# Performance work log

Hardware: AMD Instinct MI355X
Metric: run time of the kernel (lower is better)

## Reference

```python
import jax, jax.numpy as jnp
import numpy as np
from jax import lax

DN = ('NHWC', 'HWIO', 'NHWC')
EPS = 1e-7


def squash(s, axis=-1):
    sq = jnp.sum(s * s, axis=axis, keepdims=True)
    return s * (sq / (1.0 + sq) / jnp.sqrt(sq + EPS))


def setup_inputs() -> dict:
    key = jax.random.key(0)
    ks = jax.random.split(key, 4)
    inputs = jax.random.normal(ks[0], (2, 250, 250, 3), dtype=jnp.float32)
    conv_w = jax.random.normal(ks[1], (9, 9, 3, 256), dtype=jnp.float32) * 0.02
    conv_b = jnp.zeros((256,), dtype=jnp.float32)
    pc_w = jax.random.normal(ks[2], (9, 9, 256, 128), dtype=jnp.float32) * 0.02
    pc_b = jnp.zeros((128,), dtype=jnp.float32)
    # CapsLayer routing weights: [num_caps=8, in_caps=219024, dim_caps=8, in_dim=8]
    W_caps = jax.random.normal(ks[3], (8, 219024, 8, 8), dtype=jnp.float32) * 0.05
    return {"inputs": inputs, "conv_w": conv_w, "conv_b": conv_b,
            "pc_w": pc_w, "pc_b": pc_b, "W_caps": W_caps}


def reference(inputs, conv_w, conv_b, pc_w, pc_b, W_caps):
    ROUTINGS = 3
    B = inputs.shape[0]
    # Conv backbone: 250x250x3 -> 242x242x256, ReLU
    x = lax.conv_general_dilated(inputs, conv_w, (1, 1), 'VALID', dimension_numbers=DN)
    x = jax.nn.relu(x + conv_b)
    # PrimaryCaps: linear conv (128 ch, k=9, s=2, valid) -> 117x117x128 -> [B, 219024, 8] -> squash
    pc = lax.conv_general_dilated(x, pc_w, (2, 2), 'VALID', dimension_numbers=DN) + pc_b
    u = squash(pc.reshape(B, -1, 8))  # [B, N=219024, 8]
    # Prediction vectors u_hat[b,j,i,o] = W[j,i,o,d] u[b,i,d]
    u_hat = jnp.einsum('jiod,bid->bjio', W_caps, u)  # [B, J, N, 8]
    J, N = W_caps.shape[0], W_caps.shape[1]
    b_logits = jnp.zeros((B, J, N), dtype=u_hat.dtype)
    v = None
    for r in range(ROUTINGS):
        c = jax.nn.softmax(b_logits, axis=1)          # coupling over output caps
        s = jnp.einsum('bji,bjio->bjo', c, u_hat)     # [B, J, 8]
        v = squash(s)
        if r < ROUTINGS - 1:
            b_logits = b_logits + jnp.einsum('bjo,bjio->bji', v, u_hat)
    return v  # [B, 8, 8]
```

## Files before the change

### kernel.cpp

```cpp
#include <hip/hip_runtime.h>

#define N_CAPS 219024
#define J_CAPS 8

typedef __attribute__((ext_vector_type(8))) __bf16 bf16x8;
typedef __attribute__((ext_vector_type(4))) float  f32x4;
typedef __attribute__((ext_vector_type(8))) short  short8;

__device__ __forceinline__ unsigned short f2bf(float f) {
    unsigned int u = __float_as_uint(f);
    u = (u + 0x7FFFu + ((u >> 16) & 1u)) >> 16;
    return (unsigned short)u;
}

__global__ __launch_bounds__(256) void conv1_kernel(
    const float* __restrict__ in, const float* __restrict__ w,
    const float* __restrict__ bias, unsigned short* __restrict__ out)
{
    const int oc  = threadIdx.x;
    const int ox0 = blockIdx.x * 16;
    const int oy  = blockIdx.y;
    const int b   = blockIdx.z;

    __shared__ float lin[9][24][3];
    for (int idx = threadIdx.x; idx < 9 * 24 * 3; idx += 256) {
        int r   = idx / (24 * 3);
        int rem = idx - r * (24 * 3);
        int col = rem / 3;
        int c   = rem - col * 3;
        int iy  = oy + r;
        int ix  = ox0 + col;
        float v = 0.f;
        if (ix < 250) v = in[((b * 250 + iy) * 250 + ix) * 3 + c];
        lin[r][col][c] = v;
    }
    __syncthreads();

    float acc[16];
#pragma unroll
    for (int t = 0; t < 16; ++t) acc[t] = 0.f;

    for (int ky = 0; ky < 9; ++ky) {
#pragma unroll
        for (int ic = 0; ic < 3; ++ic) {
            float xv[24];
#pragma unroll
            for (int c2 = 0; c2 < 24; ++c2) xv[c2] = lin[ky][c2][ic];
#pragma unroll
            for (int kx = 0; kx < 9; ++kx) {
                float wv = w[((ky * 9 + kx) * 3 + ic) * 256 + oc];
#pragma unroll
                for (int t = 0; t < 16; ++t)
                    acc[t] += xv[kx + t] * wv;
            }
        }
    }

    float bv = bias[oc];
#pragma unroll
    for (int t = 0; t < 16; ++t) {
        int ox = ox0 + t;
        if (ox < 242) {
            float v = acc[t] + bv;
            out[((b * 242 + oy) * 242 + ox) * 256 + oc] = f2bf(v > 0.f ? v : 0.f);
        }
    }
}

__global__ __launch_bounds__(256) void w2_convert_kernel(
    const float* __restrict__ w, unsigned short* __restrict__ wt)
{
    int idx = blockIdx.x * 256 + threadIdx.x;
    if (idx >= 81 * 128 * 256) return;
    int ic = idx & 255;
    int t  = idx >> 8;
    int oc = t & 127;
    int p  = t >> 7;
    wt[idx] = f2bf(w[(p * 256 + ic) * 128 + oc]);
}

__global__ __launch_bounds__(256) void conv2_mfma_kernel(
    const unsigned short* __restrict__ x1bf,
    const unsigned short* __restrict__ w2t,
    const float* __restrict__ bias,
    float* __restrict__ out)
{
    const int bx   = blockIdx.x;
    const int oy   = blockIdx.y;
    const int b    = blockIdx.z;
    const int tid  = threadIdx.x;
    const int wave = tid >> 6;
    const int lane = tid & 63;
    const int li   = lane & 15;
    const int quad = lane >> 4;
    const int wn   = wave * 32;
    const int ox0  = bx * 64;

    __shared__ __align__(16) unsigned short As[135 * 128];

    f32x4 acc[4][2];
#pragma unroll
    for (int mt = 0; mt < 4; ++mt) {
        acc[mt][0] = (f32x4){0.f, 0.f, 0.f, 0.f};
        acc[mt][1] = (f32x4){0.f, 0.f, 0.f, 0.f};
    }

    const int n0 = wn + li;
    const int n1 = wn + 16 + li;
    const size_t bofs0 = (size_t)n0 * 256 + quad * 8;
    const size_t bofs1 = (size_t)n1 * 256 + quad * 8;

    for (int ky = 0; ky < 9; ++ky) {
        const int iy = 2 * oy + ky;
        const unsigned short* xrow =
            x1bf + ((size_t)(b * 242 + iy) * 242 + 2 * ox0) * 256;

        for (int hq = 0; hq < 2; ++hq) {
            __syncthreads();
            for (int it = 0; it < 9; ++it) {
                int ct = it * 256 + tid;
                if (ct < 135 * 16) {
                    int col = ct >> 4;
                    int cc  = ct & 15;
                    int src = cc ^ ((col >> 1) & 7);
                    *(short8*)&As[ct * 8] =
                        *(const short8*)&xrow[col * 256 + hq * 128 + src * 8];
                }
            }
            __syncthreads();

            const size_t bo0 = bofs0 + hq * 128;
            const size_t bo1 = bofs1 + hq * 128;

            for (int kx = 0; kx < 9; ++kx) {
                const unsigned short* wp = w2t + ((size_t)(ky * 9 + kx) << 15);
                const int colbase = (li << 1) + kx;
                const int sw = (li + (kx >> 1)) & 7;
                const unsigned short* abase = As + colbase * 128;
#pragma unroll
                for (int kc = 0; kc < 4; ++kc) {
                    bf16x8 b0 = *(const bf16x8*)&wp[bo0 + kc * 32];
                    bf16x8 b1 = *(const bf16x8*)&wp[bo1 + kc * 32];
                    const int chs = ((kc << 2) + quad) ^ sw;
#pragma unroll
                    for (int mt = 0; mt < 4; ++mt) {
                        bf16x8 a = *(const bf16x8*)&abase[mt * 4096 + chs * 8];
                        acc[mt][0] = __builtin_amdgcn_mfma_f32_16x16x32_bf16(a, b0, acc[mt][0], 0, 0, 0);
                        acc[mt][1] = __builtin_amdgcn_mfma_f32_16x16x32_bf16(a, b1, acc[mt][1], 0, 0, 0);
                    }
                }
            }
        }
    }

    const float bv0 = bias[n0];
    const float bv1 = bias[n1];
#pragma unroll
    for (int mt = 0; mt < 4; ++mt) {
#pragma unroll
        for (int r = 0; r < 4; ++r) {
            const int m  = mt * 16 + quad * 4 + r;
            const int ox = ox0 + m;
            if (ox < 117) {
                float* op = &out[((size_t)(b * 117 + oy) * 117 + ox) * 128];
                op[n0] = acc[mt][0][r] + bv0;
                op[n1] = acc[mt][1][r] + bv1;
            }
        }
    }
}

__global__ __launch_bounds__(256) void squash_u_kernel(float* data, int n_groups)
{
    int i = blockIdx.x * 256 + threadIdx.x;
    if (i >= n_groups) return;
    float4* p = (float4*)(data + (size_t)i * 8);
    float4 a = p[0], c = p[1];
    float sq = a.x * a.x + a.y * a.y + a.z * a.z + a.w * a.w
             + c.x * c.x + c.y * c.y + c.z * c.z + c.w * c.w;
    float scale = (sq / (1.f + sq)) * rsqrtf(sq + 1e-7f);
    p[0] = make_float4(a.x * scale, a.y * scale, a.z * scale, a.w * scale);
    p[1] = make_float4(c.x * scale, c.y * scale, c.z * scale, c.w * scale);
}

__global__ __launch_bounds__(256) void uhat_kernel(
    const float* __restrict__ W, const float* __restrict__ u,
    float* __restrict__ uhat)
{
    int idx = blockIdx.x * 256 + threadIdx.x;
    if (idx >= J_CAPS * N_CAPS) return;
    int j = idx / N_CAPS;
    int i = idx - j * N_CAPS;

    const float4* wp = (const float4*)(W + (size_t)idx * 64);
    const float4* u0 = (const float4*)(u + (size_t)i * 8);
    const float4* u1 = (const float4*)(u + ((size_t)N_CAPS + i) * 8);
    float4 u0a = u0[0], u0b = u0[1];
    float4 u1a = u1[0], u1b = u1[1];

    float o0[8], o1[8];
#pragma unroll
    for (int o = 0; o < 8; ++o) {
        float4 wa = wp[2 * o], wb = wp[2 * o + 1];
        o0[o] = wa.x * u0a.x + wa.y * u0a.y + wa.z * u0a.z + wa.w * u0a.w
              + wb.x * u0b.x + wb.y * u0b.y + wb.z * u0b.z + wb.w * u0b.w;
        o1[o] = wa.x * u1a.x + wa.y * u1a.y + wa.z * u1a.z + wa.w * u1a.w
              + wb.x * u1b.x + wb.y * u1b.y + wb.z * u1b.z + wb.w * u1b.w;
    }
    float4* d0 = (float4*)(uhat + ((size_t)(0 * J_CAPS + j) * N_CAPS + i) * 8);
    float4* d1 = (float4*)(uhat + ((size_t)(1 * J_CAPS + j) * N_CAPS + i) * 8);
    d0[0] = make_float4(o0[0], o0[1], o0[2], o0[3]);
    d0[1] = make_float4(o0[4], o0[5], o0[6], o0[7]);
    d1[0] = make_float4(o1[0], o1[1], o1[2], o1[3]);
    d1[1] = make_float4(o1[4], o1[5], o1[6], o1[7]);
}

template <int MODE>
__global__ __launch_bounds__(256) void routing_kernel(
    const float* __restrict__ uhat, const float* __restrict__ vprev,
    const float* __restrict__ b_in, float* __restrict__ b_out,
    float* __restrict__ s)
{
    const int bb = blockIdx.y;
    __shared__ float vsh[64];
    __shared__ float ssh[64];
    if (threadIdx.x < 64) {
        ssh[threadIdx.x] = 0.f;
        vsh[threadIdx.x] = (MODE > 0) ? vprev[bb * 64 + threadIdx.x] : 0.f;
    }
    __syncthreads();

    float acc[64];
#pragma unroll
    for (int k = 0; k < 64; ++k) acc[k] = 0.f;

    const float* ub = uhat + (size_t)bb * J_CAPS * (size_t)N_CAPS * 8;
    for (int i = blockIdx.x * 256 + threadIdx.x; i < N_CAPS; i += gridDim.x * 256) {
        float uh[64];
#pragma unroll
        for (int j = 0; j < 8; ++j) {
            const float* p = ub + ((size_t)j * N_CAPS + i) * 8;
            float4 x0 = *(const float4*)p;
            float4 x1 = *(const float4*)(p + 4);
            uh[j * 8 + 0] = x0.x; uh[j * 8 + 1] = x0.y;
            uh[j * 8 + 2] = x0.z; uh[j * 8 + 3] = x0.w;
            uh[j * 8 + 4] = x1.x; uh[j * 8 + 5] = x1.y;
            uh[j * 8 + 6] = x1.z; uh[j * 8 + 7] = x1.w;
        }
        float c[8];
        if (MODE == 0) {
#pragma unroll
            for (int j = 0; j < 8; ++j) c[j] = 0.125f;
        } else {
            float bj[8];
#pragma unroll
            for (int j = 0; j < 8; ++j) {
                float d = 0.f;
#pragma unroll
                for (int o = 0; o < 8; ++o) d += vsh[j * 8 + o] * uh[j * 8 + o];
                bj[j] = d;
            }
            if (MODE == 2) {
#pragma unroll
                for (int j = 0; j < 8; ++j)
                    bj[j] += b_in[((size_t)bb * 8 + j) * N_CAPS + i];
            } else {
#pragma unroll
                for (int j = 0; j < 8; ++j)
                    b_out[((size_t)bb * 8 + j) * N_CAPS + i] = bj[j];
            }
            float m = bj[0];
#pragma unroll
            for (int j = 1; j < 8; ++j) m = fmaxf(m, bj[j]);
            float se = 0.f;
#pragma unroll
            for (int j = 0; j < 8; ++j) { c[j] = __expf(bj[j] - m); se += c[j]; }
            float inv = 1.f / se;
#pragma unroll
            for (int j = 0; j < 8; ++j) c[j] *= inv;
        }
#pragma unroll
        for (int k = 0; k < 64; ++k) acc[k] += c[k >> 3] * uh[k];
    }

#pragma unroll
    for (int k = 0; k < 64; ++k) {
        float v = acc[k];
        for (int off = 32; off > 0; off >>= 1)
            v += __shfl_down(v, off, 64);
        if ((threadIdx.x & 63) == 0) atomicAdd(&ssh[k], v);
    }
    __syncthreads();
    if (threadIdx.x < 64) atomicAdd(&s[bb * 64 + threadIdx.x], ssh[threadIdx.x]);
}

__global__ void squash_v_kernel(const float* __restrict__ s, float* __restrict__ v)
{
    int t = threadIdx.x;
    if (t >= 16) return;
    const float4* p = (const float4*)(s + t * 8);
    float4 a = p[0], c = p[1];
    float sq = a.x * a.x + a.y * a.y + a.z * a.z + a.w * a.w
             + c.x * c.x + c.y * c.y + c.z * c.z + c.w * c.w;
    float scale = (sq / (1.f + sq)) * rsqrtf(sq + 1e-7f);
    float4* d = (float4*)(v + t * 8);
    d[0] = make_float4(a.x * scale, a.y * scale, a.z * scale, a.w * scale);
    d[1] = make_float4(c.x * scale, c.y * scale, c.z * scale, c.w * scale);
}

__global__ void zero_kernel(float* p, int n)
{
    int i = blockIdx.x * 256 + threadIdx.x;
    if (i < n) p[i] = 0.f;
}

extern "C" void kernel_launch(void* const* d_in, const int* in_sizes, int n_in,
                              void* d_out, int out_size, void* d_ws, size_t ws_size,
                              hipStream_t stream)
{
    const float* in = (const float*)d_in[0];
    const float* w1 = (const float*)d_in[1];
    const float* b1 = (const float*)d_in[2];
    const float* w2 = (const float*)d_in[3];
    const float* b2 = (const float*)d_in[4];
    const float* Wc = (const float*)d_in[5];
    float* out = (float*)d_out;
    char* wsb  = (char*)d_ws;

    float*          uhat = (float*)wsb;
    unsigned short* x1bf = (unsigned short*)wsb;
    float*          pc   = (float*)(wsb + 112140288);
    float*          blog = (float*)(wsb + 126157824);
    unsigned short* w2t  = (unsigned short*)(wsb + 140175360);
    float*          sbuf = (float*)(wsb + 145483776);
    float*          vbuf = (float*)(wsb + 145484288);

    w2_convert_kernel<<<(81 * 128 * 256 + 255) / 256, 256, 0, stream>>>(w2, w2t);
    conv1_kernel<<<dim3(16, 242, 2), 256, 0, stream>>>(in, w1, b1, x1bf);
    conv2_mfma_kernel<<<dim3(2, 117, 2), 256, 0, stream>>>(x1bf, w2t, b2, pc);
    squash_u_kernel<<<(2 * N_CAPS + 255) / 256, 256, 0, stream>>>(pc, 2 * N_CAPS);
    uhat_kernel<<<(J_CAPS * N_CAPS + 255) / 256, 256, 0, stream>>>(Wc, pc, uhat);

    zero_kernel<<<1, 128, 0, stream>>>(sbuf, 128);
    routing_kernel<0><<<dim3(256, 2), 256, 0, stream>>>(uhat, nullptr, nullptr, nullptr, sbuf);
    squash_v_kernel<<<1, 64, 0, stream>>>(sbuf, vbuf);

    zero_kernel<<<1, 128, 0, stream>>>(sbuf, 128);
    routing_kernel<1><<<dim3(256, 2), 256, 0, stream>>>(uhat, vbuf, nullptr, blog, sbuf);
    squash_v_kernel<<<1, 64, 0, stream>>>(sbuf, vbuf);

    zero_kernel<<<1, 128, 0, stream>>>(sbuf, 128);
    routing_kernel<2><<<dim3(256, 2), 256, 0, stream>>>(uhat, vbuf, blog, nullptr, sbuf);
    squash_v_kernel<<<1, 64, 0, stream>>>(sbuf, out);
}
```

Measured before the change: 1.305 ms.

## Split conv2 reduction over ky into three partials and widen per-wave N tile

```diff
diff --git a/kernel.cpp b/kernel.cpp
--- a/kernel.cpp
+++ b/kernel.cpp
@@ -79,13 +79,14 @@
     wt[idx] = f2bf(w[(p * 256 + ic) * 128 + oc]);
 }
 
-__global__ __launch_bounds__(256) void conv2_mfma_kernel(
+__global__ __launch_bounds__(128, 2) void conv2_mfma_kernel(
     const unsigned short* __restrict__ x1bf,
     const unsigned short* __restrict__ w2t,
-    const float* __restrict__ bias,
-    float* __restrict__ out)
+    float* __restrict__ part)
 {
     const int bx   = blockIdx.x;
+    const int oxt  = bx & 1;
+    const int kys  = bx >> 1;
     const int oy   = blockIdx.y;
     const int b    = blockIdx.z;
     const int tid  = threadIdx.x;
@@ -93,32 +94,34 @@
     const int lane = tid & 63;
     const int li   = lane & 15;
     const int quad = lane >> 4;
-    const int wn   = wave * 32;
-    const int ox0  = bx * 64;
+    const int wn   = wave * 64;
+    const int ox0  = oxt * 64;
+    const int ky0  = kys * 3;
 
     __shared__ __align__(16) unsigned short As[135 * 128];
 
-    f32x4 acc[4][2];
-#pragma unroll
-    for (int mt = 0; mt < 4; ++mt) {
-        acc[mt][0] = (f32x4){0.f, 0.f, 0.f, 0.f};
-        acc[mt][1] = (f32x4){0.f, 0.f, 0.f, 0.f};
-    }
-
-    const int n0 = wn + li;
-    const int n1 = wn + 16 + li;
-    const size_t bofs0 = (size_t)n0 * 256 + quad * 8;
-    const size_t bofs1 = (size_t)n1 * 256 + quad * 8;
-
-    for (int ky = 0; ky < 9; ++ky) {
+    f32x4 acc[4][4];
+#pragma unroll
+    for (int mt = 0; mt < 4; ++mt)
+#pragma unroll
+        for (int nt = 0; nt < 4; ++nt)
+            acc[mt][nt] = (f32x4){0.f, 0.f, 0.f, 0.f};
+
+    size_t bofs[4];
+#pragma unroll
+    for (int nt = 0; nt < 4; ++nt)
+        bofs[nt] = (size_t)(wn + nt * 16 + li) * 256 + quad * 8;
+
+    for (int kk = 0; kk < 3; ++kk) {
+        const int ky = ky0 + kk;
         const int iy = 2 * oy + ky;
         const unsigned short* xrow =
             x1bf + ((size_t)(b * 242 + iy) * 242 + 2 * ox0) * 256;
 
         for (int hq = 0; hq < 2; ++hq) {
             __syncthreads();
-            for (int it = 0; it < 9; ++it) {
-                int ct = it * 256 + tid;
+            for (int it = 0; it < 17; ++it) {
+                int ct = it * 128 + tid;
                 if (ct < 135 * 16) {
                     int col = ct >> 4;
                     int cc  = ct & 15;
@@ -129,58 +132,82 @@
             }
             __syncthreads();
 
-            const size_t bo0 = bofs0 + hq * 128;
-            const size_t bo1 = bofs1 + hq * 128;
-
             for (int kx = 0; kx < 9; ++kx) {
-                const unsigned short* wp = w2t + ((size_t)(ky * 9 + kx) << 15);
-                const int colbase = (li << 1) + kx;
+                const unsigned short* wp =
+                    w2t + ((size_t)(ky * 9 + kx) << 15) + hq * 128;
                 const int sw = (li + (kx >> 1)) & 7;
-                const unsigned short* abase = As + colbase * 128;
+                const unsigned short* abase = As + (2 * li + kx) * 128;
 #pragma unroll
                 for (int kc = 0; kc < 4; ++kc) {
-                    bf16x8 b0 = *(const bf16x8*)&wp[bo0 + kc * 32];
-                    bf16x8 b1 = *(const bf16x8*)&wp[bo1 + kc * 32];
+                    bf16x8 bfr[4];
+#pragma unroll
+                    for (int nt = 0; nt < 4; ++nt)
+                        bfr[nt] = *(const bf16x8*)&wp[bofs[nt] + kc * 32];
                     const int chs = ((kc << 2) + quad) ^ sw;
+                    __builtin_amdgcn_s_setprio(1);
 #pragma unroll
                     for (int mt = 0; mt < 4; ++mt) {
                         bf16x8 a = *(const bf16x8*)&abase[mt * 4096 + chs * 8];
-                        acc[mt][0] = __builtin_amdgcn_mfma_f32_16x16x32_bf16(a, b0, acc[mt][0], 0, 0, 0);
-                        acc[mt][1] = __builtin_amdgcn_mfma_f32_16x16x32_bf16(a, b1, acc[mt][1], 0, 0, 0);
+#pragma unroll
+                        for (int nt = 0; nt < 4; ++nt)
+                            acc[mt][nt] = __builtin_amdgcn_mfma_f32_16x16x32_bf16(
+                                a, bfr[nt], acc[mt][nt], 0, 0, 0);
                     }
+                    __builtin_amdgcn_s_setprio(0);
                 }
             }
         }
     }
 
-    const float bv0 = bias[n0];
-    const float bv1 = bias[n1];
+    float* pp = part + (size_t)kys * (2ull * 117 * 117 * 128)
+              + (size_t)(b * 117 + oy) * 117 * 128;
 #pragma unroll
     for (int mt = 0; mt < 4; ++mt) {
 #pragma unroll
         for (int r = 0; r < 4; ++r) {
-            const int m  = mt * 16 + quad * 4 + r;
-            const int ox = ox0 + m;
+            const int ox = ox0 + mt * 16 + quad * 4 + r;
             if (ox < 117) {
-                float* op = &out[((size_t)(b * 117 + oy) * 117 + ox) * 128];
-                op[n0] = acc[mt][0][r] + bv0;
-                op[n1] = acc[mt][1][r] + bv1;
-            }
-        }
-    }
-}
-
-__global__ __launch_bounds__(256) void squash_u_kernel(float* data, int n_groups)
-{
-    int i = blockIdx.x * 256 + threadIdx.x;
-    if (i >= n_groups) return;
-    float4* p = (float4*)(data + (size_t)i * 8);
-    float4 a = p[0], c = p[1];
-    float sq = a.x * a.x + a.y * a.y + a.z * a.z + a.w * a.w
-             + c.x * c.x + c.y * c.y + c.z * c.z + c.w * c.w;
+                float* op = pp + (size_t)ox * 128 + li;
+                op[wn]      = acc[mt][0][r];
+                op[wn + 16] = acc[mt][1][r];
+                op[wn + 32] = acc[mt][2][r];
+                op[wn + 48] = acc[mt][3][r];
+            }
+        }
+    }
+}
+
+__global__ __launch_bounds__(256) void squash_u_kernel(
+    const float* __restrict__ part, const float* __restrict__ bias,
+    float* __restrict__ u, int n_groups)
+{
+    int g = blockIdx.x * 256 + threadIdx.x;
+    if (g >= n_groups) return;
+    const size_t PSZ = 2ull * 117 * 117 * 128;
+    const float4* p0 = (const float4*)(part + (size_t)g * 8);
+    const float4* p1 = (const float4*)(part + PSZ + (size_t)g * 8);
+    const float4* p2 = (const float4*)(part + 2 * PSZ + (size_t)g * 8);
+    const float4* bp = (const float4*)(bias + (g & 15) * 8);
+    float4 a0 = p0[0], c0 = p0[1];
+    float4 a1 = p1[0], c1 = p1[1];
+    float4 a2 = p2[0], c2 = p2[1];
+    float4 ba = bp[0], bc = bp[1];
+    float x[8];
+    x[0] = a0.x + a1.x + a2.x + ba.x;
+    x[1] = a0.y + a1.y + a2.y + ba.y;
+    x[2] = a0.z + a1.z + a2.z + ba.z;
+    x[3] = a0.w + a1.w + a2.w + ba.w;
+    x[4] = c0.x + c1.x + c2.x + bc.x;
+    x[5] = c0.y + c1.y + c2.y + bc.y;
+    x[6] = c0.z + c1.z + c2.z + bc.z;
+    x[7] = c0.w + c1.w + c2.w + bc.w;
+    float sq = 0.f;
+#pragma unroll
+    for (int j = 0; j < 8; ++j) sq += x[j] * x[j];
     float scale = (sq / (1.f + sq)) * rsqrtf(sq + 1e-7f);
-    p[0] = make_float4(a.x * scale, a.y * scale, a.z * scale, a.w * scale);
-    p[1] = make_float4(c.x * scale, c.y * scale, c.z * scale, c.w * scale);
+    float4* d = (float4*)(u + (size_t)g * 8);
+    d[0] = make_float4(x[0] * scale, x[1] * scale, x[2] * scale, x[3] * scale);
+    d[1] = make_float4(x[4] * scale, x[5] * scale, x[6] * scale, x[7] * scale);
 }
 
 __global__ __launch_bounds__(256) void uhat_kernel(
@@ -327,18 +354,19 @@
     float* out = (float*)d_out;
     char* wsb  = (char*)d_ws;
 
-    float*          uhat = (float*)wsb;
-    unsigned short* x1bf = (unsigned short*)wsb;
-    float*          pc   = (float*)(wsb + 112140288);
-    float*          blog = (float*)(wsb + 126157824);
-    unsigned short* w2t  = (unsigned short*)(wsb + 140175360);
-    float*          sbuf = (float*)(wsb + 145483776);
-    float*          vbuf = (float*)(wsb + 145484288);
+    float*          uhat   = (float*)wsb;
+    unsigned short* x1bf   = (unsigned short*)wsb;
+    float*          pcpart = (float*)(wsb + 59969536);
+    float*          pc     = (float*)(wsb + 112140288);
+    float*          blog   = (float*)(wsb + 126157824);
+    unsigned short* w2t    = (unsigned short*)(wsb + 140175360);
+    float*          sbuf   = (float*)(wsb + 145483776);
+    float*          vbuf   = (float*)(wsb + 145484288);
 
     w2_convert_kernel<<<(81 * 128 * 256 + 255) / 256, 256, 0, stream>>>(w2, w2t);
     conv1_kernel<<<dim3(16, 242, 2), 256, 0, stream>>>(in, w1, b1, x1bf);
-    conv2_mfma_kernel<<<dim3(2, 117, 2), 256, 0, stream>>>(x1bf, w2t, b2, pc);
-    squash_u_kernel<<<(2 * N_CAPS + 255) / 256, 256, 0, stream>>>(pc, 2 * N_CAPS);
+    conv2_mfma_kernel<<<dim3(6, 117, 2), 128, 0, stream>>>(x1bf, w2t, pcpart);
+    squash_u_kernel<<<(2 * N_CAPS + 255) / 256, 256, 0, stream>>>(pcpart, b2, pc, 2 * N_CAPS);
     uhat_kernel<<<(J_CAPS * N_CAPS + 255) / 256, 256, 0, stream>>>(Wc, pc, uhat);
 
     zero_kernel<<<1, 128, 0, stream>>>(sbuf, 128);
```

After: 1.397 ms. +7.1%, slower.

## Double-buffer conv2 input tiles with async global-to-LDS loads

Applied to the files above, without the earlier changes.

```diff
diff --git a/kernel.cpp b/kernel.cpp
--- a/kernel.cpp
+++ b/kernel.cpp
@@ -6,6 +6,9 @@
 typedef __attribute__((ext_vector_type(8))) __bf16 bf16x8;
 typedef __attribute__((ext_vector_type(4))) float  f32x4;
 typedef __attribute__((ext_vector_type(8))) short  short8;
+
+typedef const __attribute__((address_space(1))) unsigned int gld_t;
+typedef __attribute__((address_space(3))) unsigned int lds_t;
 
 __device__ __forceinline__ unsigned short f2bf(float f) {
     unsigned int u = __float_as_uint(f);
@@ -79,7 +82,7 @@
     wt[idx] = f2bf(w[(p * 256 + ic) * 128 + oc]);
 }
 
-__global__ __launch_bounds__(256) void conv2_mfma_kernel(
+__global__ __launch_bounds__(256, 4) void conv2_mfma_kernel(
     const unsigned short* __restrict__ x1bf,
     const unsigned short* __restrict__ w2t,
     const float* __restrict__ bias,
@@ -96,7 +99,7 @@
     const int wn   = wave * 32;
     const int ox0  = bx * 64;
 
-    __shared__ __align__(16) unsigned short As[135 * 128];
+    __shared__ __align__(16) unsigned short As[2][135 * 64];
 
     f32x4 acc[4][2];
 #pragma unroll
@@ -110,47 +113,58 @@
     const size_t bofs0 = (size_t)n0 * 256 + quad * 8;
     const size_t bofs1 = (size_t)n1 * 256 + quad * 8;
 
-    for (int ky = 0; ky < 9; ++ky) {
-        const int iy = 2 * oy + ky;
-        const unsigned short* xrow =
-            x1bf + ((size_t)(b * 242 + iy) * 242 + 2 * ox0) * 256;
-
-        for (int hq = 0; hq < 2; ++hq) {
-            __syncthreads();
-            for (int it = 0; it < 9; ++it) {
-                int ct = it * 256 + tid;
-                if (ct < 135 * 16) {
-                    int col = ct >> 4;
-                    int cc  = ct & 15;
-                    int src = cc ^ ((col >> 1) & 7);
-                    *(short8*)&As[ct * 8] =
-                        *(const short8*)&xrow[col * 256 + hq * 128 + src * 8];
+    const unsigned short* xbase =
+        x1bf + ((size_t)(b * 242 + 2 * oy) * 242 + 2 * ox0) * 256;
+
+    auto stage = [&](int p) {
+        const int ky = p >> 2;
+        const int q  = p & 3;
+        const unsigned short* xr = xbase + (size_t)ky * (242 * 256) + q * 64;
+        unsigned short* db = &As[p & 1][0];
+#pragma unroll
+        for (int it = 0; it < 5; ++it) {
+            int ct = it * 256 + tid;
+            if (ct < 135 * 8) {
+                int col = ct >> 3;
+                int cc  = ct & 7;
+                int src = cc ^ ((col >> 1) & 7);
+                __builtin_amdgcn_global_load_lds(
+                    (gld_t*)(xr + (size_t)col * 256 + src * 8),
+                    (lds_t*)(db + (size_t)(it * 256 + wave * 64) * 8),
+                    16, 0, 0);
+            }
+        }
+    };
+
+    stage(0);
+    __syncthreads();
+
+    for (int p = 0; p < 36; ++p) {
+        if (p < 35) stage(p + 1);
+
+        const int ky = p >> 2;
+        const int q  = p & 3;
+        const unsigned short* asb = As[p & 1];
+
+        for (int kx = 0; kx < 9; ++kx) {
+            const unsigned short* wp =
+                w2t + ((size_t)(ky * 9 + kx) << 15) + q * 64;
+            const int sw = (li + (kx >> 1)) & 7;
+            const int colb = 2 * li + kx;
+#pragma unroll
+            for (int kc = 0; kc < 2; ++kc) {
+                bf16x8 b0 = *(const bf16x8*)&wp[bofs0 + kc * 32];
+                bf16x8 b1 = *(const bf16x8*)&wp[bofs1 + kc * 32];
+                const int c4 = ((kc << 2) + quad) ^ sw;
+#pragma unroll
+                for (int mt = 0; mt < 4; ++mt) {
+                    bf16x8 a = *(const bf16x8*)&asb[(size_t)(mt * 32 + colb) * 64 + c4 * 8];
+                    acc[mt][0] = __builtin_amdgcn_mfma_f32_16x16x32_bf16(a, b0, acc[mt][0], 0, 0, 0);
+                    acc[mt][1] = __builtin_amdgcn_mfma_f32_16x16x32_bf16(a, b1, acc[mt][1], 0, 0, 0);
                 }
             }
-            __syncthreads();
-
-            const size_t bo0 = bofs0 + hq * 128;
-            const size_t bo1 = bofs1 + hq * 128;
-
-            for (int kx = 0; kx < 9; ++kx) {
-                const unsigned short* wp = w2t + ((size_t)(ky * 9 + kx) << 15);
-                const int colbase = (li << 1) + kx;
-                const int sw = (li + (kx >> 1)) & 7;
-                const unsigned short* abase = As + colbase * 128;
-#pragma unroll
-                for (int kc = 0; kc < 4; ++kc) {
-                    bf16x8 b0 = *(const bf16x8*)&wp[bo0 + kc * 32];
-                    bf16x8 b1 = *(const bf16x8*)&wp[bo1 + kc * 32];
-                    const int chs = ((kc << 2) + quad) ^ sw;
-#pragma unroll
-                    for (int mt = 0; mt < 4; ++mt) {
-                        bf16x8 a = *(const bf16x8*)&abase[mt * 4096 + chs * 8];
-                        acc[mt][0] = __builtin_amdgcn_mfma_f32_16x16x32_bf16(a, b0, acc[mt][0], 0, 0, 0);
-                        acc[mt][1] = __builtin_amdgcn_mfma_f32_16x16x32_bf16(a, b1, acc[mt][1], 0, 0, 0);
-                    }
-                }
-            }
-        }
+        }
+        __syncthreads();
     }
 
     const float bv0 = bias[n0];
```

Measured after the change: 1.271 ms. 1.03x faster.
